# Kernel optimization log

Hardware: AMD Instinct MI355X
Metric: run time of the kernel (lower is better)

Reference implementation:

```python
import jax, jax.numpy as jnp
import numpy as np

B, S, D, H = 2, 2048, 1024, 16
HD = D // H
FF = 4 * D
EPS = 1e-5


def _layernorm(x, g, b):
    m = jnp.mean(x, axis=-1, keepdims=True)
    v = jnp.var(x, axis=-1, keepdims=True)
    return (x - m) * jax.lax.rsqrt(v + EPS) * g + b


def setup_inputs() -> dict:
    key = jax.random.key(0)
    ks = jax.random.split(key, 13)
    s = lambda fan_in: 1.0 / np.sqrt(fan_in)
    return {
        "x": jax.random.normal(ks[0], (B, S, D), jnp.float32),
        "ln1_g": jnp.ones((D,), jnp.float32),
        "ln1_b": jnp.zeros((D,), jnp.float32),
        "w_qkv": jax.random.uniform(ks[1], (D, 3 * D), jnp.float32, -s(D), s(D)),
        "b_qkv": jax.random.uniform(ks[2], (3 * D,), jnp.float32, -s(D), s(D)),
        "w_proj": jax.random.uniform(ks[3], (D, D), jnp.float32, -s(D), s(D)),
        "b_proj": jax.random.uniform(ks[4], (D,), jnp.float32, -s(D), s(D)),
        "ln2_g": jnp.ones((D,), jnp.float32),
        "ln2_b": jnp.zeros((D,), jnp.float32),
        "w_fc1": jax.random.uniform(ks[5], (D, FF), jnp.float32, -s(D), s(D)),
        "b_fc1": jax.random.uniform(ks[6], (FF,), jnp.float32, -s(D), s(D)),
        "w_fc2": jax.random.uniform(ks[7], (FF, D), jnp.float32, -s(FF), s(FF)),
        "b_fc2": jax.random.uniform(ks[8], (D,), jnp.float32, -s(FF), s(FF)),
    }


def reference(x, ln1_g, ln1_b, w_qkv, b_qkv, w_proj, b_proj,
              ln2_g, ln2_b, w_fc1, b_fc1, w_fc2, b_fc2):
    scale = 1.0 / np.sqrt(HD)
    # pre-LN attention
    h = _layernorm(x, ln1_g, ln1_b)
    qkv = h @ w_qkv + b_qkv                                # [B,S,3D]
    qkv = qkv.reshape(B, S, 3, H, HD).transpose(2, 0, 3, 1, 4)
    q, k, v = qkv[0], qkv[1], qkv[2]                       # [B,H,S,HD]
    scores = jnp.einsum("bhqd,bhkd->bhqk", q, k) * scale   # [B,H,S,S]
    causal = jnp.tril(jnp.ones((S, S), bool))
    scores = jnp.where(causal, scores, -jnp.inf)
    attn = jax.nn.softmax(scores, axis=-1)
    out = jnp.einsum("bhqk,bhkd->bhqd", attn, v)           # [B,H,S,HD]
    out = out.transpose(0, 2, 1, 3).reshape(B, S, D)
    out = out @ w_proj + b_proj
    x = x + out
    # pre-LN MLP
    h = _layernorm(x, ln2_g, ln2_b)
    h = jax.nn.gelu(h @ w_fc1 + b_fc1, approximate=False)
    h = h @ w_fc2 + b_fc2
    return x + h
```

## Files before the change

### kernel.cpp

```cpp
#include <hip/hip_runtime.h>
#include <hip/hip_bf16.h>

#define BDIM 1024
#define SEQ  2048
#define NB   2
#define NH   16
#define HDIM 64
#define FFDIM 4096
#define MROWS (NB*SEQ)

typedef __attribute__((ext_vector_type(8))) short short8;
typedef __attribute__((ext_vector_type(4))) float f32x4;

static __device__ __forceinline__ unsigned short f2bf(float f) {
  union { float f; unsigned u; } v; v.f = f;
  unsigned r = v.u + 0x7fffu + ((v.u >> 16) & 1u);
  return (unsigned short)(r >> 16);
}

static __device__ __forceinline__ f32x4 splat4(float x) {
  f32x4 v; v[0] = x; v[1] = x; v[2] = x; v[3] = x; return v;
}

#define GLOAD16(gp, lp)                                                        \
  __builtin_amdgcn_global_load_lds(                                            \
      (const __attribute__((address_space(1))) void*)(gp),                     \
      (__attribute__((address_space(3))) void*)(lp), 16, 0, 0)

__global__ void tcvt_all(const float* __restrict__ w0, const float* __restrict__ w1,
                         const float* __restrict__ w2, const float* __restrict__ w3,
                         unsigned short* __restrict__ o0, unsigned short* __restrict__ o1,
                         unsigned short* __restrict__ o2, unsigned short* __restrict__ o3) {
  const int bid = blockIdx.x;
  const float* in; unsigned short* out; int R, C, nbx, rem;
  if (bid < 3072)      { in = w0; out = o0; R = 1024; C = 3072; rem = bid;        nbx = 96;  }
  else if (bid < 4096) { in = w1; out = o1; R = 1024; C = 1024; rem = bid - 3072; nbx = 32;  }
  else if (bid < 8192) { in = w2; out = o2; R = 1024; C = 4096; rem = bid - 4096; nbx = 128; }
  else                 { in = w3; out = o3; R = 4096; C = 1024; rem = bid - 8192; nbx = 32;  }
  const int c0 = (rem % nbx) * 32, r0 = (rem / nbx) * 32;
  __shared__ float tile[32][36];
  const int t = threadIdx.x;
  {
    const int row = t >> 3, col4 = (t & 7) * 4;
    const float4 v = *(const float4*)(in + (size_t)(r0 + row) * C + c0 + col4);
    *(float4*)&tile[row][col4] = v;
  }
  __syncthreads();
  {
    const int c = t & 31, rg = t >> 5;
    ushort4 o;
    o.x = f2bf(tile[rg * 4 + 0][c]);
    o.y = f2bf(tile[rg * 4 + 1][c]);
    o.z = f2bf(tile[rg * 4 + 2][c]);
    o.w = f2bf(tile[rg * 4 + 3][c]);
    *(ushort4*)(out + (size_t)(c0 + c) * R + r0 + rg * 4) = o;
  }
}

__global__ void vtr_kernel(const unsigned short* __restrict__ qkv,
                           unsigned short* __restrict__ vt) {
  __shared__ unsigned short tile[32][72];
  const int h = blockIdx.z & 15, b = blockIdx.z >> 4;
  const int s0 = blockIdx.y * 64, d0 = blockIdx.x * 32;
  const int t = threadIdx.x;
  const unsigned short* src = qkv + (size_t)b * SEQ * 3072 + 2048 + h * HDIM + d0;
  {
    const int s = t & 63, d8 = (t >> 6) * 8;
    const short8 v = *(const short8*)(src + (size_t)(s0 + s) * 3072 + d8);
#pragma unroll
    for (int j = 0; j < 8; ++j) tile[d8 + j][s] = (unsigned short)v[j];
  }
  __syncthreads();
  {
    const int d = t >> 3, s8 = (t & 7) * 8;
    const short8 v = *(const short8*)&tile[d][s8];
    *(short8*)(vt + (size_t)(b * NH + h) * HDIM * SEQ + (size_t)(d0 + d) * SEQ + s0 + s8) = v;
  }
}

__global__ void ln_kernel(const float* __restrict__ x, const float* __restrict__ g,
                          const float* __restrict__ b, unsigned short* __restrict__ out) {
  const int row = blockIdx.x;
  const int tid = threadIdx.x;
  const float4 v = ((const float4*)(x + (size_t)row * BDIM))[tid];
  float s  = v.x + v.y + v.z + v.w;
  float ss = v.x * v.x + v.y * v.y + v.z * v.z + v.w * v.w;
#pragma unroll
  for (int off = 32; off; off >>= 1) { s += __shfl_xor(s, off); ss += __shfl_xor(ss, off); }
  __shared__ float red[8];
  const int wave = tid >> 6;
  if ((tid & 63) == 0) { red[wave * 2] = s; red[wave * 2 + 1] = ss; }
  __syncthreads();
  s  = red[0] + red[2] + red[4] + red[6];
  ss = red[1] + red[3] + red[5] + red[7];
  const float mean = s * (1.0f / BDIM);
  const float inv  = rsqrtf(ss * (1.0f / BDIM) - mean * mean + 1e-5f);
  const float4 gg = ((const float4*)g)[tid];
  const float4 bb = ((const float4*)b)[tid];
  ushort4 o;
  o.x = f2bf((v.x - mean) * inv * gg.x + bb.x);
  o.y = f2bf((v.y - mean) * inv * gg.y + bb.y);
  o.z = f2bf((v.z - mean) * inv * gg.z + bb.z);
  o.w = f2bf((v.w - mean) * inv * gg.w + bb.w);
  ((ushort4*)(out + (size_t)row * BDIM))[tid] = o;
}

template <int EPI>
__global__ __launch_bounds__(256, 3)
void gemm_bt(const unsigned short* __restrict__ A, const unsigned short* __restrict__ Bt,
             const float* __restrict__ bias, const float* __restrict__ resid,
             void* __restrict__ outp, int M, int N, int K) {
  __shared__ unsigned short As[128 * 32];
  __shared__ unsigned short Bs[128 * 32];
  const int tid = threadIdx.x;
  const int n0 = blockIdx.x * 128, m0 = blockIdx.y * 128;
  const int lane = tid & 63, wave = tid >> 6;
  const int lr = lane & 15, lg = lane >> 4;
  const int wr = (wave >> 1) * 64, wc = (wave & 1) * 64;

  const unsigned short* ga0 = A  + (size_t)(m0 + (tid >> 2)) * K + (tid & 3) * 8;
  const unsigned short* ga1 = ga0 + (size_t)64 * K;
  const unsigned short* gb0 = Bt + (size_t)(n0 + (tid >> 2)) * K + (tid & 3) * 8;
  const unsigned short* gb1 = gb0 + (size_t)64 * K;
  unsigned short* la0 = As + tid * 8;
  unsigned short* la1 = As + (256 + tid) * 8;
  unsigned short* lb0 = Bs + tid * 8;
  unsigned short* lb1 = Bs + (256 + tid) * 8;

  f32x4 acc[4][4];
#pragma unroll
  for (int i = 0; i < 4; i++)
#pragma unroll
    for (int j = 0; j < 4; j++) acc[i][j] = splat4(0.0f);

  for (int k0 = 0; k0 < K; k0 += 32) {
    GLOAD16(ga0 + k0, la0);
    GLOAD16(ga1 + k0, la1);
    GLOAD16(gb0 + k0, lb0);
    GLOAD16(gb1 + k0, lb1);
    __syncthreads();
    short8 af[4], bfr[4];
#pragma unroll
    for (int mi = 0; mi < 4; mi++)
      af[mi] = *(const short8*)(As + (wr + mi * 16 + lr) * 32 + lg * 8);
#pragma unroll
    for (int ni = 0; ni < 4; ni++)
      bfr[ni] = *(const short8*)(Bs + (wc + ni * 16 + lr) * 32 + lg * 8);
#pragma unroll
    for (int mi = 0; mi < 4; mi++)
#pragma unroll
      for (int ni = 0; ni < 4; ni++)
        acc[mi][ni] = __builtin_amdgcn_mfma_f32_16x16x32_bf16(af[mi], bfr[ni], acc[mi][ni], 0, 0, 0);
    __syncthreads();
  }

  float bv[4];
#pragma unroll
  for (int ni = 0; ni < 4; ni++) bv[ni] = bias[n0 + wc + ni * 16 + lr];
#pragma unroll
  for (int mi = 0; mi < 4; mi++) {
#pragma unroll
    for (int ni = 0; ni < 4; ni++) {
      const int row0 = m0 + wr + mi * 16 + lg * 4;
      const int col  = n0 + wc + ni * 16 + lr;
#pragma unroll
      for (int r = 0; r < 4; r++) {
        const float v = acc[mi][ni][r] + bv[ni];
        const size_t idx = (size_t)(row0 + r) * N + col;
        if constexpr (EPI == 0) {
          ((unsigned short*)outp)[idx] = f2bf(v);
        } else if constexpr (EPI == 1) {
          ((float*)outp)[idx] = v + resid[idx];
        } else {
          const float t = 0.5f * v * (1.0f + erff(v * 0.70710678118f));
          ((unsigned short*)outp)[idx] = f2bf(t);
        }
      }
    }
  }
}

__global__ __launch_bounds__(256, 3)
void gemm_bt_n64(const unsigned short* __restrict__ A, const unsigned short* __restrict__ Bt,
                 const float* __restrict__ bias, const float* __restrict__ resid,
                 float* __restrict__ outp, int M, int N, int K) {
  __shared__ unsigned short As[128 * 32];
  __shared__ unsigned short Bs[64 * 32];
  const int tid = threadIdx.x;
  const int n0 = blockIdx.x * 64, m0 = blockIdx.y * 128;
  const int lane = tid & 63, wave = tid >> 6;
  const int lr = lane & 15, lg = lane >> 4;
  const int wr = wave * 32;

  const unsigned short* ga0 = A  + (size_t)(m0 + (tid >> 2)) * K + (tid & 3) * 8;
  const unsigned short* ga1 = ga0 + (size_t)64 * K;
  const unsigned short* gb0 = Bt + (size_t)(n0 + (tid >> 2)) * K + (tid & 3) * 8;
  unsigned short* la0 = As + tid * 8;
  unsigned short* la1 = As + (256 + tid) * 8;
  unsigned short* lb0 = Bs + tid * 8;

  f32x4 acc[2][4];
#pragma unroll
  for (int i = 0; i < 2; i++)
#pragma unroll
    for (int j = 0; j < 4; j++) acc[i][j] = splat4(0.0f);

  for (int k0 = 0; k0 < K; k0 += 32) {
    GLOAD16(ga0 + k0, la0);
    GLOAD16(ga1 + k0, la1);
    GLOAD16(gb0 + k0, lb0);
    __syncthreads();
    short8 af[2], bfr[4];
#pragma unroll
    for (int mi = 0; mi < 2; mi++)
      af[mi] = *(const short8*)(As + (wr + mi * 16 + lr) * 32 + lg * 8);
#pragma unroll
    for (int ni = 0; ni < 4; ni++)
      bfr[ni] = *(const short8*)(Bs + (ni * 16 + lr) * 32 + lg * 8);
#pragma unroll
    for (int mi = 0; mi < 2; mi++)
#pragma unroll
      for (int ni = 0; ni < 4; ni++)
        acc[mi][ni] = __builtin_amdgcn_mfma_f32_16x16x32_bf16(af[mi], bfr[ni], acc[mi][ni], 0, 0, 0);
    __syncthreads();
  }

  float bv[4];
#pragma unroll
  for (int ni = 0; ni < 4; ni++) bv[ni] = bias[n0 + ni * 16 + lr];
#pragma unroll
  for (int mi = 0; mi < 2; mi++) {
#pragma unroll
    for (int ni = 0; ni < 4; ni++) {
      const int row0 = m0 + wr + mi * 16 + lg * 4;
      const int col  = n0 + ni * 16 + lr;
#pragma unroll
      for (int r = 0; r < 4; r++) {
        const size_t idx = (size_t)(row0 + r) * N + col;
        outp[idx] = acc[mi][ni][r] + bv[ni] + resid[idx];
      }
    }
  }
}

__global__ __launch_bounds__(64, 3)
void attn_kernel(const unsigned short* __restrict__ qkv,
                 const unsigned short* __restrict__ vT,
                 unsigned short* __restrict__ out) {
  __shared__ unsigned short psw[32 * 72];
  const int lane = threadIdx.x & 63;
  const int lr = lane & 15, lg = lane >> 4;
  const int wq0 = blockIdx.x * 32;
  const int h = blockIdx.y, bb = blockIdx.z;
  const size_t base = (size_t)bb * SEQ * 3072;
  const unsigned short* kb_g = qkv + base + 1024 + h * HDIM;
  const unsigned short* vth = vT + (size_t)(bb * NH + h) * HDIM * SEQ;
  const float SC = 0.125f * 1.44269504089f;

  short8 qf[2][2];
#pragma unroll
  for (int qb = 0; qb < 2; ++qb)
#pragma unroll
    for (int kc = 0; kc < 2; ++kc)
      qf[qb][kc] = *(const short8*)(qkv + base +
          (size_t)(wq0 + qb * 16 + lr) * 3072 + h * HDIM + kc * 32 + lg * 8);

  f32x4 oacc[2][4];
#pragma unroll
  for (int qb = 0; qb < 2; ++qb)
#pragma unroll
    for (int n = 0; n < 4; ++n) oacc[qb][n] = splat4(0.0f);
  f32x4 m_i[2] = { splat4(-INFINITY), splat4(-INFINITY) };
  f32x4 l_i[2] = { splat4(0.0f), splat4(0.0f) };

  const int TB = wq0 / 64 + 1;

  for (int t = 0; t < TB; ++t) {
    const int kk = t * 64;
    short8 kf[4][2];
#pragma unroll
    for (int kb = 0; kb < 4; ++kb)
#pragma unroll
      for (int kc = 0; kc < 2; ++kc)
        kf[kb][kc] = *(const short8*)(kb_g + (size_t)(kk + kb * 16 + lr) * 3072 +
                                      kc * 32 + lg * 8);
    f32x4 s[2][4];
#pragma unroll
    for (int qb = 0; qb < 2; ++qb)
#pragma unroll
      for (int kb = 0; kb < 4; ++kb) s[qb][kb] = splat4(0.0f);
    __builtin_amdgcn_s_setprio(1);
#pragma unroll
    for (int qb = 0; qb < 2; ++qb)
#pragma unroll
      for (int kb = 0; kb < 4; ++kb) {
        s[qb][kb] = __builtin_amdgcn_mfma_f32_16x16x32_bf16(qf[qb][0], kf[kb][0], s[qb][kb], 0, 0, 0);
        s[qb][kb] = __builtin_amdgcn_mfma_f32_16x16x32_bf16(qf[qb][1], kf[kb][1], s[qb][kb], 0, 0, 0);
      }
    __builtin_amdgcn_s_setprio(0);

    const bool nm = (kk + 64 > wq0);
#pragma unroll
    for (int qb = 0; qb < 2; ++qb)
#pragma unroll
      for (int kb = 0; kb < 4; ++kb)
#pragma unroll
        for (int r = 0; r < 4; ++r) {
          float v = s[qb][kb][r] * SC;
          if (nm) {
            const int q = wq0 + qb * 16 + lg * 4 + r;
            if (kk + kb * 16 + lr > q) v = -INFINITY;
          }
          s[qb][kb][r] = v;
        }

    f32x4 mx[2];
#pragma unroll
    for (int qb = 0; qb < 2; ++qb)
#pragma unroll
      for (int r = 0; r < 4; ++r)
        mx[qb][r] = fmaxf(fmaxf(s[qb][0][r], s[qb][1][r]),
                          fmaxf(s[qb][2][r], s[qb][3][r]));
#pragma unroll
    for (int msk = 1; msk < 16; msk <<= 1)
#pragma unroll
      for (int qb = 0; qb < 2; ++qb)
#pragma unroll
        for (int r = 0; r < 4; ++r)
          mx[qb][r] = fmaxf(mx[qb][r], __shfl_xor(mx[qb][r], msk));
    f32x4 mnew[2], corr[2];
#pragma unroll
    for (int qb = 0; qb < 2; ++qb)
#pragma unroll
      for (int r = 0; r < 4; ++r) {
        mnew[qb][r] = fmaxf(m_i[qb][r], mx[qb][r]);
        corr[qb][r] = exp2f(m_i[qb][r] - mnew[qb][r]);
      }
#pragma unroll
    for (int qb = 0; qb < 2; ++qb)
#pragma unroll
      for (int kb = 0; kb < 4; ++kb)
#pragma unroll
        for (int r = 0; r < 4; ++r)
          s[qb][kb][r] = exp2f(s[qb][kb][r] - mnew[qb][r]);
    f32x4 ps[2];
#pragma unroll
    for (int qb = 0; qb < 2; ++qb)
#pragma unroll
      for (int r = 0; r < 4; ++r)
        ps[qb][r] = (s[qb][0][r] + s[qb][1][r]) + (s[qb][2][r] + s[qb][3][r]);
#pragma unroll
    for (int msk = 1; msk < 16; msk <<= 1)
#pragma unroll
      for (int qb = 0; qb < 2; ++qb)
#pragma unroll
        for (int r = 0; r < 4; ++r)
          ps[qb][r] += __shfl_xor(ps[qb][r], msk);
#pragma unroll
    for (int qb = 0; qb < 2; ++qb)
#pragma unroll
      for (int r = 0; r < 4; ++r) {
        l_i[qb][r] = l_i[qb][r] * corr[qb][r] + ps[qb][r];
        m_i[qb][r] = mnew[qb][r];
      }
#pragma unroll
    for (int qb = 0; qb < 2; ++qb)
#pragma unroll
      for (int n = 0; n < 4; ++n)
#pragma unroll
        for (int r = 0; r < 4; ++r) oacc[qb][n][r] *= corr[qb][r];

#pragma unroll
    for (int qb = 0; qb < 2; ++qb)
#pragma unroll
      for (int kb = 0; kb < 4; ++kb)
#pragma unroll
        for (int r = 0; r < 4; ++r)
          psw[(qb * 16 + lg * 4 + r) * 72 + kb * 16 + lr] = f2bf(s[qb][kb][r]);

    short8 pf[2][2], vf[4][2];
#pragma unroll
    for (int qb = 0; qb < 2; ++qb)
#pragma unroll
      for (int kc = 0; kc < 2; ++kc)
        pf[qb][kc] = *(const short8*)(psw + (qb * 16 + lr) * 72 + kc * 32 + lg * 8);
#pragma unroll
    for (int n = 0; n < 4; ++n)
#pragma unroll
      for (int kc = 0; kc < 2; ++kc)
        vf[n][kc] = *(const short8*)(vth + (size_t)(n * 16 + lr) * SEQ +
                                     kk + kc * 32 + lg * 8);
    __builtin_amdgcn_s_setprio(1);
#pragma unroll
    for (int qb = 0; qb < 2; ++qb)
#pragma unroll
      for (int n = 0; n < 4; ++n) {
        oacc[qb][n] = __builtin_amdgcn_mfma_f32_16x16x32_bf16(pf[qb][0], vf[n][0], oacc[qb][n], 0, 0, 0);
        oacc[qb][n] = __builtin_amdgcn_mfma_f32_16x16x32_bf16(pf[qb][1], vf[n][1], oacc[qb][n], 0, 0, 0);
      }
    __builtin_amdgcn_s_setprio(0);
  }

  f32x4 linv[2];
#pragma unroll
  for (int qb = 0; qb < 2; ++qb)
#pragma unroll
    for (int r = 0; r < 4; ++r) linv[qb][r] = 1.0f / l_i[qb][r];
#pragma unroll
  for (int qb = 0; qb < 2; ++qb)
#pragma unroll
    for (int n = 0; n < 4; ++n)
#pragma unroll
      for (int r = 0; r < 4; ++r)
        out[(size_t)(bb * SEQ + wq0 + qb * 16 + lg * 4 + r) * BDIM + h * HDIM + n * 16 + lr]
            = f2bf(oacc[qb][n][r] * linv[qb][r]);
}

extern "C" void kernel_launch(void* const* d_in, const int* in_sizes, int n_in,
                              void* d_out, int out_size, void* d_ws, size_t ws_size,
                              hipStream_t stream) {
  const float* x      = (const float*)d_in[0];
  const float* ln1_g  = (const float*)d_in[1];
  const float* ln1_b  = (const float*)d_in[2];
  const float* w_qkv  = (const float*)d_in[3];
  const float* b_qkv  = (const float*)d_in[4];
  const float* w_proj = (const float*)d_in[5];
  const float* b_proj = (const float*)d_in[6];
  const float* ln2_g  = (const float*)d_in[7];
  const float* ln2_b  = (const float*)d_in[8];
  const float* w_fc1  = (const float*)d_in[9];
  const float* b_fc1  = (const float*)d_in[10];
  const float* w_fc2  = (const float*)d_in[11];
  const float* b_fc2  = (const float*)d_in[12];
  float* out = (float*)d_out;

  char* ws = (char*)d_ws;
  unsigned short* wqkvT  = (unsigned short*)(ws + 0);
  unsigned short* wprojT = (unsigned short*)(ws + 6291456);
  unsigned short* wfc1T  = (unsigned short*)(ws + 8388608);
  unsigned short* wfc2T  = (unsigned short*)(ws + 16777216);
  unsigned short* hbuf   = (unsigned short*)(ws + 25165824);
  float*          x2     = (float*)         (ws + 33554432);
  unsigned short* qkvb   = (unsigned short*)(ws + 50331648);
  unsigned short* attnb  = (unsigned short*)(ws + 75497472);
  unsigned short* fc1b   = (unsigned short*)(ws + 50331648);

  tcvt_all<<<12288, 256, 0, stream>>>(w_qkv, w_proj, w_fc1, w_fc2,
                                      wqkvT, wprojT, wfc1T, wfc2T);

  ln_kernel<<<MROWS, 256, 0, stream>>>(x, ln1_g, ln1_b, hbuf);
  gemm_bt<0><<<dim3(3072 / 128, MROWS / 128), 256, 0, stream>>>(hbuf, wqkvT, b_qkv, nullptr, qkvb, MROWS, 3072, 1024);
  vtr_kernel<<<dim3(HDIM / 32, SEQ / 64, NB * NH), 256, 0, stream>>>(qkvb, hbuf);
  attn_kernel<<<dim3(SEQ / 32, NH, NB), 64, 0, stream>>>(qkvb, hbuf, attnb);
  gemm_bt_n64<<<dim3(1024 / 64, MROWS / 128), 256, 0, stream>>>(attnb, wprojT, b_proj, x, x2, MROWS, 1024, 1024);

  ln_kernel<<<MROWS, 256, 0, stream>>>(x2, ln2_g, ln2_b, hbuf);
  gemm_bt<2><<<dim3(4096 / 128, MROWS / 128), 256, 0, stream>>>(hbuf, wfc1T, b_fc1, nullptr, fc1b, MROWS, FFDIM, 1024);
  gemm_bt_n64<<<dim3(1024 / 64, MROWS / 128), 256, 0, stream>>>(fc1b, wfc2T, b_fc2, x2, out, MROWS, 1024, FFDIM);
}
```

Baseline: 465.5 us.

## Share K/V tiles in LDS across four waves with causal load-balanced query blocks

Attention now runs 256-thread blocks in which four waves, each owning 32 query rows, share K and V tiles staged cooperatively into XOR-swizzled LDS. Before, each 64-thread wave read K and V directly from global memory. Each block handles query block p and its mirror 15-p, so every block does the same amount of causal work, and the grid is a flat 256 blocks with heads interleaved. This cuts redundant global K/V traffic and evens out the causal imbalance. In exchange it adds two __syncthreads per tile, the loads are not double-buffered, and there are fewer, larger blocks.

```diff
diff --git a/kernel.cpp b/kernel.cpp
--- a/kernel.cpp
+++ b/kernel.cpp
@@ -243,177 +243,205 @@
   }
 }
 
-__global__ __launch_bounds__(64, 3)
+__global__ __launch_bounds__(256, 2)
 void attn_kernel(const unsigned short* __restrict__ qkv,
                  const unsigned short* __restrict__ vT,
                  unsigned short* __restrict__ out) {
-  __shared__ unsigned short psw[32 * 72];
-  const int lane = threadIdx.x & 63;
+  __shared__ unsigned short Ks[64 * 64];
+  __shared__ unsigned short Vs[64 * 64];
+  __shared__ unsigned short Ps[4][32 * 72];
+  const int tid = threadIdx.x;
+  const int wave = tid >> 6, lane = tid & 63;
   const int lr = lane & 15, lg = lane >> 4;
-  const int wq0 = blockIdx.x * 32;
-  const int h = blockIdx.y, bb = blockIdx.z;
+  const int id = blockIdx.x;
+  const int bh = (id & 7) | (((id >> 3) & 3) << 3);
+  const int p  = id >> 5;
+  const int h = bh & 15, bb = bh >> 4;
   const size_t base = (size_t)bb * SEQ * 3072;
-  const unsigned short* kb_g = qkv + base + 1024 + h * HDIM;
-  const unsigned short* vth = vT + (size_t)(bb * NH + h) * HDIM * SEQ;
+  const unsigned short* vth = vT + (size_t)bh * HDIM * SEQ;
+  unsigned short* psw = Ps[wave];
+  const int sw = lr & 7;
   const float SC = 0.125f * 1.44269504089f;
 
-  short8 qf[2][2];
-#pragma unroll
-  for (int qb = 0; qb < 2; ++qb)
-#pragma unroll
-    for (int kc = 0; kc < 2; ++kc)
-      qf[qb][kc] = *(const short8*)(qkv + base +
-          (size_t)(wq0 + qb * 16 + lr) * 3072 + h * HDIM + kc * 32 + lg * 8);
-
-  f32x4 oacc[2][4];
-#pragma unroll
-  for (int qb = 0; qb < 2; ++qb)
-#pragma unroll
-    for (int n = 0; n < 4; ++n) oacc[qb][n] = splat4(0.0f);
-  f32x4 m_i[2] = { splat4(-INFINITY), splat4(-INFINITY) };
-  f32x4 l_i[2] = { splat4(0.0f), splat4(0.0f) };
-
-  const int TB = wq0 / 64 + 1;
-
-  for (int t = 0; t < TB; ++t) {
-    const int kk = t * 64;
-    short8 kf[4][2];
-#pragma unroll
-    for (int kb = 0; kb < 4; ++kb)
+  const int srow = tid >> 3;
+  const int scb  = (tid & 7) ^ (srow & 7);
+  const unsigned short* kg0 = qkv + base + (size_t)srow * 3072 + 1024 + h * HDIM + scb * 8;
+  const unsigned short* vg0 = vth + (size_t)srow * SEQ + scb * 8;
+  unsigned short* kl0 = Ks + tid * 8;
+  unsigned short* kl1 = Ks + 2048 + tid * 8;
+  unsigned short* vl0 = Vs + tid * 8;
+  unsigned short* vl1 = Vs + 2048 + tid * 8;
+
+#pragma unroll 1
+  for (int half = 0; half < 2; ++half) {
+    const int qblk = half ? (15 - p) : p;
+    const int Q0 = qblk * 128;
+    const int wq0 = Q0 + wave * 32;
+    const int TB = qblk * 2 + 2;
+
+    short8 qf[2][2];
+#pragma unroll
+    for (int qb = 0; qb < 2; ++qb)
 #pragma unroll
       for (int kc = 0; kc < 2; ++kc)
-        kf[kb][kc] = *(const short8*)(kb_g + (size_t)(kk + kb * 16 + lr) * 3072 +
-                                      kc * 32 + lg * 8);
-    f32x4 s[2][4];
+        qf[qb][kc] = *(const short8*)(qkv + base +
+            (size_t)(wq0 + qb * 16 + lr) * 3072 + h * HDIM + kc * 32 + lg * 8);
+
+    f32x4 oacc[2][4];
 #pragma unroll
     for (int qb = 0; qb < 2; ++qb)
 #pragma unroll
-      for (int kb = 0; kb < 4; ++kb) s[qb][kb] = splat4(0.0f);
-    __builtin_amdgcn_s_setprio(1);
+      for (int n = 0; n < 4; ++n) oacc[qb][n] = splat4(0.0f);
+    f32x4 m_i[2] = { splat4(-INFINITY), splat4(-INFINITY) };
+    f32x4 l_i[2] = { splat4(0.0f), splat4(0.0f) };
+
+    for (int t = 0; t < TB; ++t) {
+      const int kk = t * 64;
+      __syncthreads();
+      GLOAD16(kg0 + (size_t)kk * 3072, kl0);
+      GLOAD16(kg0 + (size_t)(kk + 32) * 3072, kl1);
+      GLOAD16(vg0 + kk, vl0);
+      GLOAD16(vg0 + (size_t)32 * SEQ + kk, vl1);
+      __syncthreads();
+
+      short8 kf[4][2];
+#pragma unroll
+      for (int kb = 0; kb < 4; ++kb)
+#pragma unroll
+        for (int kc = 0; kc < 2; ++kc)
+          kf[kb][kc] = *(const short8*)(Ks + (kb * 16 + lr) * 64 +
+                                        (((kc * 4 + lg) ^ sw) * 8));
+      f32x4 s[2][4];
+#pragma unroll
+      for (int qb = 0; qb < 2; ++qb)
+#pragma unroll
+        for (int kb = 0; kb < 4; ++kb) s[qb][kb] = splat4(0.0f);
+      __builtin_amdgcn_s_setprio(1);
+#pragma unroll
+      for (int qb = 0; qb < 2; ++qb)
+#pragma unroll
+        for (int kb = 0; kb < 4; ++kb) {
+          s[qb][kb] = __builtin_amdgcn_mfma_f32_16x16x32_bf16(qf[qb][0], kf[kb][0], s[qb][kb], 0, 0, 0);
+          s[qb][kb] = __builtin_amdgcn_mfma_f32_16x16x32_bf16(qf[qb][1], kf[kb][1], s[qb][kb], 0, 0, 0);
+        }
+      __builtin_amdgcn_s_setprio(0);
+
+      const bool nm = (kk + 64 > wq0);
+#pragma unroll
+      for (int qb = 0; qb < 2; ++qb)
+#pragma unroll
+        for (int kb = 0; kb < 4; ++kb)
+#pragma unroll
+          for (int r = 0; r < 4; ++r) {
+            float v = s[qb][kb][r] * SC;
+            if (nm) {
+              const int q = wq0 + qb * 16 + lg * 4 + r;
+              if (kk + kb * 16 + lr > q) v = -INFINITY;
+            }
+            s[qb][kb][r] = v;
+          }
+
+      f32x4 mx[2];
+#pragma unroll
+      for (int qb = 0; qb < 2; ++qb)
+#pragma unroll
+        for (int r = 0; r < 4; ++r)
+          mx[qb][r] = fmaxf(fmaxf(s[qb][0][r], s[qb][1][r]),
+                            fmaxf(s[qb][2][r], s[qb][3][r]));
+#pragma unroll
+      for (int msk = 1; msk < 16; msk <<= 1)
+#pragma unroll
+        for (int qb = 0; qb < 2; ++qb)
+#pragma unroll
+          for (int r = 0; r < 4; ++r)
+            mx[qb][r] = fmaxf(mx[qb][r], __shfl_xor(mx[qb][r], msk));
+      f32x4 mnew[2], corr[2];
+#pragma unroll
+      for (int qb = 0; qb < 2; ++qb)
+#pragma unroll
+        for (int r = 0; r < 4; ++r) {
+          mnew[qb][r] = fmaxf(m_i[qb][r], mx[qb][r]);
+          corr[qb][r] = exp2f(m_i[qb][r] - mnew[qb][r]);
+        }
+#pragma unroll
+      for (int qb = 0; qb < 2; ++qb)
+#pragma unroll
+        for (int kb = 0; kb < 4; ++kb)
+#pragma unroll
+          for (int r = 0; r < 4; ++r)
+            s[qb][kb][r] = exp2f(s[qb][kb][r] - mnew[qb][r]);
+      f32x4 ps[2];
+#pragma unroll
+      for (int qb = 0; qb < 2; ++qb)
+#pragma unroll
+        for (int r = 0; r < 4; ++r)
+          ps[qb][r] = (s[qb][0][r] + s[qb][1][r]) + (s[qb][2][r] + s[qb][3][r]);
+#pragma unroll
+      for (int msk = 1; msk < 16; msk <<= 1)
+#pragma unroll
+        for (int qb = 0; qb < 2; ++qb)
+#pragma unroll
+          for (int r = 0; r < 4; ++r)
+            ps[qb][r] += __shfl_xor(ps[qb][r], msk);
+#pragma unroll
+      for (int qb = 0; qb < 2; ++qb)
+#pragma unroll
+        for (int r = 0; r < 4; ++r) {
+          l_i[qb][r] = l_i[qb][r] * corr[qb][r] + ps[qb][r];
+          m_i[qb][r] = mnew[qb][r];
+        }
+#pragma unroll
+      for (int qb = 0; qb < 2; ++qb)
+#pragma unroll
+        for (int n = 0; n < 4; ++n)
+#pragma unroll
+          for (int r = 0; r < 4; ++r) oacc[qb][n][r] *= corr[qb][r];
+
+#pragma unroll
+      for (int qb = 0; qb < 2; ++qb)
+#pragma unroll
+        for (int kb = 0; kb < 4; ++kb)
+#pragma unroll
+          for (int r = 0; r < 4; ++r)
+            psw[(qb * 16 + lg * 4 + r) * 72 + kb * 16 + lr] = f2bf(s[qb][kb][r]);
+
+      short8 pf[2][2], vf[4][2];
+#pragma unroll
+      for (int qb = 0; qb < 2; ++qb)
+#pragma unroll
+        for (int kc = 0; kc < 2; ++kc)
+          pf[qb][kc] = *(const short8*)(psw + (qb * 16 + lr) * 72 + kc * 32 + lg * 8);
+#pragma unroll
+      for (int n = 0; n < 4; ++n)
+#pragma unroll
+        for (int kc = 0; kc < 2; ++kc)
+          vf[n][kc] = *(const short8*)(Vs + (n * 16 + lr) * 64 +
+                                       (((kc * 4 + lg) ^ sw) * 8));
+      __builtin_amdgcn_s_setprio(1);
+#pragma unroll
+      for (int qb = 0; qb < 2; ++qb)
+#pragma unroll
+        for (int n = 0; n < 4; ++n) {
+          oacc[qb][n] = __builtin_amdgcn_mfma_f32_16x16x32_bf16(pf[qb][0], vf[n][0], oacc[qb][n], 0, 0, 0);
+          oacc[qb][n] = __builtin_amdgcn_mfma_f32_16x16x32_bf16(pf[qb][1], vf[n][1], oacc[qb][n], 0, 0, 0);
+        }
+      __builtin_amdgcn_s_setprio(0);
+    }
+
+    f32x4 linv[2];
 #pragma unroll
     for (int qb = 0; qb < 2; ++qb)
 #pragma unroll
-      for (int kb = 0; kb < 4; ++kb) {
-        s[qb][kb] = __builtin_amdgcn_mfma_f32_16x16x32_bf16(qf[qb][0], kf[kb][0], s[qb][kb], 0, 0, 0);
-        s[qb][kb] = __builtin_amdgcn_mfma_f32_16x16x32_bf16(qf[qb][1], kf[kb][1], s[qb][kb], 0, 0, 0);
-      }
-    __builtin_amdgcn_s_setprio(0);
-
-    const bool nm = (kk + 64 > wq0);
+      for (int r = 0; r < 4; ++r) linv[qb][r] = 1.0f / l_i[qb][r];
 #pragma unroll
     for (int qb = 0; qb < 2; ++qb)
 #pragma unroll
-      for (int kb = 0; kb < 4; ++kb)
-#pragma unroll
-        for (int r = 0; r < 4; ++r) {
-          float v = s[qb][kb][r] * SC;
-          if (nm) {
-            const int q = wq0 + qb * 16 + lg * 4 + r;
-            if (kk + kb * 16 + lr > q) v = -INFINITY;
-          }
-          s[qb][kb][r] = v;
-        }
-
-    f32x4 mx[2];
-#pragma unroll
-    for (int qb = 0; qb < 2; ++qb)
-#pragma unroll
-      for (int r = 0; r < 4; ++r)
-        mx[qb][r] = fmaxf(fmaxf(s[qb][0][r], s[qb][1][r]),
-                          fmaxf(s[qb][2][r], s[qb][3][r]));
-#pragma unroll
-    for (int msk = 1; msk < 16; msk <<= 1)
-#pragma unroll
-      for (int qb = 0; qb < 2; ++qb)
+      for (int n = 0; n < 4; ++n)
 #pragma unroll
         for (int r = 0; r < 4; ++r)
-          mx[qb][r] = fmaxf(mx[qb][r], __shfl_xor(mx[qb][r], msk));
-    f32x4 mnew[2], corr[2];
-#pragma unroll
-    for (int qb = 0; qb < 2; ++qb)
-#pragma unroll
-      for (int r = 0; r < 4; ++r) {
-        mnew[qb][r] = fmaxf(m_i[qb][r], mx[qb][r]);
-        corr[qb][r] = exp2f(m_i[qb][r] - mnew[qb][r]);
-      }
-#pragma unroll
-    for (int qb = 0; qb < 2; ++qb)
-#pragma unroll
-      for (int kb = 0; kb < 4; ++kb)
-#pragma unroll
-        for (int r = 0; r < 4; ++r)
-          s[qb][kb][r] = exp2f(s[qb][kb][r] - mnew[qb][r]);
-    f32x4 ps[2];
-#pragma unroll
-    for (int qb = 0; qb < 2; ++qb)
-#pragma unroll
-      for (int r = 0; r < 4; ++r)
-        ps[qb][r] = (s[qb][0][r] + s[qb][1][r]) + (s[qb][2][r] + s[qb][3][r]);
-#pragma unroll
-    for (int msk = 1; msk < 16; msk <<= 1)
-#pragma unroll
-      for (int qb = 0; qb < 2; ++qb)
-#pragma unroll
-        for (int r = 0; r < 4; ++r)
-          ps[qb][r] += __shfl_xor(ps[qb][r], msk);
-#pragma unroll
-    for (int qb = 0; qb < 2; ++qb)
-#pragma unroll
-      for (int r = 0; r < 4; ++r) {
-        l_i[qb][r] = l_i[qb][r] * corr[qb][r] + ps[qb][r];
-        m_i[qb][r] = mnew[qb][r];
-      }
-#pragma unroll
-    for (int qb = 0; qb < 2; ++qb)
-#pragma unroll
-      for (int n = 0; n < 4; ++n)
-#pragma unroll
-        for (int r = 0; r < 4; ++r) oacc[qb][n][r] *= corr[qb][r];
-
-#pragma unroll
-    for (int qb = 0; qb < 2; ++qb)
-#pragma unroll
-      for (int kb = 0; kb < 4; ++kb)
-#pragma unroll
-        for (int r = 0; r < 4; ++r)
-          psw[(qb * 16 + lg * 4 + r) * 72 + kb * 16 + lr] = f2bf(s[qb][kb][r]);
-
-    short8 pf[2][2], vf[4][2];
-#pragma unroll
-    for (int qb = 0; qb < 2; ++qb)
-#pragma unroll
-      for (int kc = 0; kc < 2; ++kc)
-        pf[qb][kc] = *(const short8*)(psw + (qb * 16 + lr) * 72 + kc * 32 + lg * 8);
-#pragma unroll
-    for (int n = 0; n < 4; ++n)
-#pragma unroll
-      for (int kc = 0; kc < 2; ++kc)
-        vf[n][kc] = *(const short8*)(vth + (size_t)(n * 16 + lr) * SEQ +
-                                     kk + kc * 32 + lg * 8);
-    __builtin_amdgcn_s_setprio(1);
-#pragma unroll
-    for (int qb = 0; qb < 2; ++qb)
-#pragma unroll
-      for (int n = 0; n < 4; ++n) {
-        oacc[qb][n] = __builtin_amdgcn_mfma_f32_16x16x32_bf16(pf[qb][0], vf[n][0], oacc[qb][n], 0, 0, 0);
-        oacc[qb][n] = __builtin_amdgcn_mfma_f32_16x16x32_bf16(pf[qb][1], vf[n][1], oacc[qb][n], 0, 0, 0);
-      }
-    __builtin_amdgcn_s_setprio(0);
-  }
-
-  f32x4 linv[2];
-#pragma unroll
-  for (int qb = 0; qb < 2; ++qb)
-#pragma unroll
-    for (int r = 0; r < 4; ++r) linv[qb][r] = 1.0f / l_i[qb][r];
-#pragma unroll
-  for (int qb = 0; qb < 2; ++qb)
-#pragma unroll
-    for (int n = 0; n < 4; ++n)
-#pragma unroll
-      for (int r = 0; r < 4; ++r)
-        out[(size_t)(bb * SEQ + wq0 + qb * 16 + lg * 4 + r) * BDIM + h * HDIM + n * 16 + lr]
-            = f2bf(oacc[qb][n][r] * linv[qb][r]);
+          out[(size_t)(bb * SEQ + wq0 + qb * 16 + lg * 4 + r) * BDIM + h * HDIM + n * 16 + lr]
+              = f2bf(oacc[qb][n][r] * linv[qb][r]);
+  }
 }
 
 extern "C" void kernel_launch(void* const* d_in, const int* in_sizes, int n_in,
@@ -451,7 +479,7 @@
   ln_kernel<<<MROWS, 256, 0, stream>>>(x, ln1_g, ln1_b, hbuf);
   gemm_bt<0><<<dim3(3072 / 128, MROWS / 128), 256, 0, stream>>>(hbuf, wqkvT, b_qkv, nullptr, qkvb, MROWS, 3072, 1024);
   vtr_kernel<<<dim3(HDIM / 32, SEQ / 64, NB * NH), 256, 0, stream>>>(qkvb, hbuf);
-  attn_kernel<<<dim3(SEQ / 32, NH, NB), 64, 0, stream>>>(qkvb, hbuf, attnb);
+  attn_kernel<<<256, 256, 0, stream>>>(qkvb, hbuf, attnb);
   gemm_bt_n64<<<dim3(1024 / 64, MROWS / 128), 256, 0, stream>>>(attnb, wprojT, b_proj, x, x2, MROWS, 1024, 1024);
 
   ln_kernel<<<MROWS, 256, 0, stream>>>(x2, ln2_g, ln2_b, hbuf);
```

After: 422.2 us. -9.3%, faster.
